# Kernel optimization log

Measured on AMD Instinct MI355X. Metric: run time of the kernel, lower is better.

The kernel has to match this reference:

```python
import jax, jax.numpy as jnp
import numpy as np

B, N, S, VOCAB, D, NNZ = 16, 2048, 4096, 50257, 128, 1048576


def setup_inputs() -> dict:
    key = jax.random.key(0)
    k1, k2, k3, k4, k5, k6 = jax.random.split(key, 6)
    return {
        "subnode_ids": jax.random.randint(k1, (B, S), 0, VOCAB),
        "mask_batch": jax.random.randint(k2, (NNZ,), 0, B),
        "mask_node": jax.random.randint(k3, (NNZ,), 0, N),
        "mask_subnode": jax.random.randint(k4, (NNZ,), 0, S),
        "mask_values": jax.random.uniform(k5, (NNZ,), dtype=jnp.float32),
        "emb_table": jax.random.normal(k6, (VOCAB, D), dtype=jnp.float32),
    }


def reference(subnode_ids, mask_batch, mask_node, mask_subnode, mask_values, emb_table):
    # Gather token embeddings for every (batch, subnode) slot: [B, S, D] -> [B*S, D]
    subnode_emb = emb_table[subnode_ids].reshape(B * S, D)
    # Flattened COO indices (same as batch*max_nodes + node, batch*max_subnodes + subnode)
    row = mask_batch * N + mask_node      # destination node slot in [0, B*N)
    col = mask_batch * S + mask_subnode   # source subnode slot in [0, B*S)
    # Fused gather + weighted scatter-add (== sparse.mm of expanded_mask @ subnode_emb)
    contrib = subnode_emb[col] * mask_values[:, None]           # [NNZ, D]
    pooled = jax.ops.segment_sum(contrib, row, num_segments=B * N)  # [B*N, D]
    return pooled.reshape(B, N, D)
```

## Files before the change

### kernel.cpp

```cpp
#include <hip/hip_runtime.h>
#include <hip/hip_fp16.h>

#define Bq 16
#define Nq 2048
#define Sq 4096
#define Dq 128
#define VOCABq 50257
#define NNZq 1048576
#define ROWS (Bq * Nq)
#define NBIN 1024
#define RPB 32
#define BCAP 1280
#define OVF_MAX 65536
#define BTPB 1024
#define BEPT 4

typedef unsigned long long u64;
typedef float vfloat4 __attribute__((ext_vector_type(4)));
typedef unsigned short vushort4 __attribute__((ext_vector_type(4)));

__global__ __launch_bounds__(256) void cast_kernel(
    const float* __restrict__ emb, unsigned short* __restrict__ emb16)
{
    const int NQUAD = (VOCABq * Dq) / 4;
    int i = blockIdx.x * 256 + threadIdx.x;
    if (i >= NQUAD) return;
    vfloat4 f = reinterpret_cast<const vfloat4*>(emb)[i];
    vushort4 h;
    h.x = __half_as_ushort(__float2half_rn(f.x));
    h.y = __half_as_ushort(__float2half_rn(f.y));
    h.z = __half_as_ushort(__float2half_rn(f.z));
    h.w = __half_as_ushort(__float2half_rn(f.w));
    __builtin_nontemporal_store(h, reinterpret_cast<vushort4*>(emb16) + i);
}

__global__ __launch_bounds__(BTPB) void bin_kernel(
    const int* __restrict__ subnode_ids,
    const int* __restrict__ mb,
    const int* __restrict__ mn,
    const int* __restrict__ ms,
    const float* __restrict__ mv,
    int* __restrict__ binCnt,
    u64* __restrict__ binMem,
    int* __restrict__ ovfn,
    int* __restrict__ ovf)
{
    __shared__ int hist[NBIN];
    __shared__ int base[NBIN];
    int t = threadIdx.x;
    for (int g = t; g < NBIN; g += BTPB) hist[g] = 0;
    __syncthreads();

    int blockBase = blockIdx.x * (BTPB * BEPT);
    int g[BEPT], rank[BEPT];
    u64 pk[BEPT];
    #pragma unroll
    for (int k = 0; k < BEPT; k++) {
        int i   = blockBase + k * BTPB + t;
        int b   = mb[i];
        int row = b * Nq + mn[i];
        int tok = subnode_ids[b * Sq + ms[i]];
        float v = mv[i];
        g[k]  = row >> 5;
        pk[k] = ((u64)(unsigned)__float_as_int(v) << 32)
              | ((u64)(row & 31) << 16)
              | (unsigned)tok;
        rank[k] = atomicAdd(&hist[g[k]], 1);
    }
    __syncthreads();
    for (int gg = t; gg < NBIN; gg += BTPB) {
        int h = hist[gg];
        base[gg] = h ? atomicAdd(&binCnt[gg], h) : 0;
    }
    __syncthreads();
    #pragma unroll
    for (int k = 0; k < BEPT; k++) {
        int p = base[g[k]] + rank[k];
        if (p < BCAP) {
            binMem[(size_t)g[k] * BCAP + p] = pk[k];
        } else {
            int o = atomicAdd(ovfn, 1);
            if (o < OVF_MAX) ovf[o] = blockBase + k * BTPB + t;
        }
    }
}

__global__ __launch_bounds__(256) void pool_kernel(
    const unsigned short* __restrict__ emb16,
    const int* __restrict__ binCnt,
    const u64* __restrict__ binMem,
    float* __restrict__ out)
{
    __shared__ u64 ebuf[BCAP];
    __shared__ int hist[RPB];
    __shared__ int start[RPB + 1];
    __shared__ int cursor[RPB];

    int t   = threadIdx.x;
    int bin = blockIdx.x;
    if (t < RPB) hist[t] = 0;
    __syncthreads();

    int n = min(binCnt[bin], BCAP);
    const u64* bm = binMem + (size_t)bin * BCAP;

    for (int e = t; e < n; e += 256) {
        int rl = (int)((bm[e] >> 16) & 31);
        atomicAdd(&hist[rl], 1);
    }
    __syncthreads();
    if (t < 32) {
        int v = hist[t];
        #pragma unroll
        for (int d = 1; d < 32; d <<= 1) {
            int w = __shfl_up(v, d, 32);
            if (t >= d) v += w;
        }
        start[t + 1] = v;
        if (t == 0) start[0] = 0;
    }
    __syncthreads();
    if (t < RPB) cursor[t] = start[t];
    __syncthreads();
    for (int e = t; e < n; e += 256) {
        u64 pk = bm[e];
        int rl = (int)((pk >> 16) & 31);
        int p  = atomicAdd(&cursor[rl], 1);
        ebuf[p] = pk;
    }
    __syncthreads();

    int gi   = t >> 5;
    int lane = t & 31;
    for (int rr = 0; rr < 4; rr++) {
        int r  = gi * 4 + rr;
        int s0 = start[r], s1 = start[r + 1];
        vfloat4 acc = {0.f, 0.f, 0.f, 0.f};
        int k = s0;
        for (; k + 8 <= s1; k += 8) {
            int   tk[8];
            float vv[8];
            #pragma unroll
            for (int u = 0; u < 8; u++) {
                u64 pk = ebuf[k + u];
                tk[u] = (int)(pk & 0xFFFF);
                vv[u] = __int_as_float((int)(pk >> 32));
            }
            vushort4 e[8];
            #pragma unroll
            for (int u = 0; u < 8; u++)
                e[u] = reinterpret_cast<const vushort4*>(emb16 + (size_t)tk[u] * Dq)[lane];
            #pragma unroll
            for (int u = 0; u < 8; u++) {
                acc.x += __half2float(__ushort_as_half(e[u].x)) * vv[u];
                acc.y += __half2float(__ushort_as_half(e[u].y)) * vv[u];
                acc.z += __half2float(__ushort_as_half(e[u].z)) * vv[u];
                acc.w += __half2float(__ushort_as_half(e[u].w)) * vv[u];
            }
        }
        for (; k < s1; k++) {
            u64 pk = ebuf[k];
            int   tok = (int)(pk & 0xFFFF);
            float v   = __int_as_float((int)(pk >> 32));
            vushort4 e = reinterpret_cast<const vushort4*>(emb16 + (size_t)tok * Dq)[lane];
            acc.x += __half2float(__ushort_as_half(e.x)) * v;
            acc.y += __half2float(__ushort_as_half(e.y)) * v;
            acc.z += __half2float(__ushort_as_half(e.z)) * v;
            acc.w += __half2float(__ushort_as_half(e.w)) * v;
        }
        __builtin_nontemporal_store(
            acc, reinterpret_cast<vfloat4*>(out + ((size_t)bin * RPB + r) * Dq) + lane);
    }
}

__global__ __launch_bounds__(256) void overflow_kernel(
    const int* __restrict__ subnode_ids,
    const int* __restrict__ mb, const int* __restrict__ mn,
    const int* __restrict__ ms, const float* __restrict__ mv,
    const float* __restrict__ emb,
    const int* __restrict__ ovfn, const int* __restrict__ ovf,
    float* __restrict__ out)
{
    int nov = min(*ovfn, OVF_MAX);
    for (int e = blockIdx.x * 256 + threadIdx.x; e < nov; e += gridDim.x * 256) {
        int i = ovf[e];
        int b = mb[i];
        int row = b * Nq + mn[i];
        int tok = subnode_ids[b * Sq + ms[i]];
        float v = mv[i];
        const float* src = emb + (size_t)tok * Dq;
        float* dst = out + (size_t)row * Dq;
        for (int d = 0; d < Dq; d++) unsafeAtomicAdd(dst + d, src[d] * v);
    }
}

extern "C" void kernel_launch(void* const* d_in, const int* in_sizes, int n_in,
                              void* d_out, int out_size, void* d_ws, size_t ws_size,
                              hipStream_t stream) {
    const int*   subnode_ids  = (const int*)d_in[0];
    const int*   mask_batch   = (const int*)d_in[1];
    const int*   mask_node    = (const int*)d_in[2];
    const int*   mask_subnode = (const int*)d_in[3];
    const float* mask_values  = (const float*)d_in[4];
    const float* emb_table    = (const float*)d_in[5];
    float*       out          = (float*)d_out;

    unsigned short* emb16 = (unsigned short*)d_ws;
    u64* binMem = (u64*)(emb16 + (size_t)VOCABq * Dq + 64 );
    int* binCnt = (int*)(binMem + (size_t)NBIN * BCAP);
    int* ovfn   = binCnt + NBIN;
    int* ovf    = ovfn + 64;

    (void)hipMemsetAsync(binCnt, 0, (NBIN + 64) * sizeof(int), stream);

    const int NQUAD = (VOCABq * Dq) / 4;
    cast_kernel<<<(NQUAD + 255) / 256, 256, 0, stream>>>(emb_table, emb16);
    bin_kernel<<<NNZq / (BTPB * BEPT), BTPB, 0, stream>>>(
        subnode_ids, mask_batch, mask_node, mask_subnode, mask_values,
        binCnt, binMem, ovfn, ovf);
    pool_kernel<<<NBIN, 256, 0, stream>>>(emb16, binCnt, binMem, out);
    overflow_kernel<<<32, 256, 0, stream>>>(
        subnode_ids, mask_batch, mask_node, mask_subnode, mask_values,
        emb_table, ovfn, ovf, out);
}
```

Measured before the change: 143.2 us.

## Halve pool bin size, sort entries by token range, widen gathers to 16B

Bins now cover 16 rows instead of 32, doubling the pool grid to 2048 blocks. Inside each bin, entries are sorted by a (token high bits, row) key so that concurrent groups gather from nearby embedding regions. Each 16-lane group owns one row across the four token quarters. Gathers are widened to 8 halves per lane, and entries are kept in registers so the bin buffer is read from global memory once instead of twice. The change aims to improve occupancy, load width and L2 locality, at the cost of lower bin capacity (768), which could push more entries onto the slow atomic overflow path.

```diff
diff --git a/kernel.cpp b/kernel.cpp
--- a/kernel.cpp
+++ b/kernel.cpp
@@ -8,9 +8,9 @@
 #define VOCABq 50257
 #define NNZq 1048576
 #define ROWS (Bq * Nq)
-#define NBIN 1024
-#define RPB 32
-#define BCAP 1280
+#define NBIN 2048
+#define RPB 16
+#define BCAP 768
 #define OVF_MAX 65536
 #define BTPB 1024
 #define BEPT 4
@@ -18,6 +18,7 @@
 typedef unsigned long long u64;
 typedef float vfloat4 __attribute__((ext_vector_type(4)));
 typedef unsigned short vushort4 __attribute__((ext_vector_type(4)));
+typedef unsigned short vushort8 __attribute__((ext_vector_type(8)));
 
 __global__ __launch_bounds__(256) void cast_kernel(
     const float* __restrict__ emb, unsigned short* __restrict__ emb16)
@@ -61,9 +62,9 @@
         int row = b * Nq + mn[i];
         int tok = subnode_ids[b * Sq + ms[i]];
         float v = mv[i];
-        g[k]  = row >> 5;
+        g[k]  = row >> 4;
         pk[k] = ((u64)(unsigned)__float_as_int(v) << 32)
-              | ((u64)(row & 31) << 16)
+              | ((u64)(row & 15) << 16)
               | (unsigned)tok;
         rank[k] = atomicAdd(&hist[g[k]], 1);
     }
@@ -92,50 +93,54 @@
     float* __restrict__ out)
 {
     __shared__ u64 ebuf[BCAP];
-    __shared__ int hist[RPB];
-    __shared__ int start[RPB + 1];
-    __shared__ int cursor[RPB];
+    __shared__ int hist[64];
+    __shared__ int start[65];
+    __shared__ int cursor[64];
 
     int t   = threadIdx.x;
     int bin = blockIdx.x;
-    if (t < RPB) hist[t] = 0;
+    if (t < 64) hist[t] = 0;
     __syncthreads();
 
     int n = min(binCnt[bin], BCAP);
     const u64* bm = binMem + (size_t)bin * BCAP;
 
+    u64 myPk[3];
+    int myKey[3], myCnt = 0;
     for (int e = t; e < n; e += 256) {
-        int rl = (int)((bm[e] >> 16) & 31);
-        atomicAdd(&hist[rl], 1);
-    }
-    __syncthreads();
-    if (t < 32) {
+        u64 pk  = bm[e];
+        int tok = (int)(pk & 0xFFFF);
+        int key = ((tok >> 14) << 4) | (int)((pk >> 16) & 15);
+        myPk[myCnt] = pk; myKey[myCnt] = key; myCnt++;
+        atomicAdd(&hist[key], 1);
+    }
+    __syncthreads();
+    if (t < 64) {
         int v = hist[t];
         #pragma unroll
-        for (int d = 1; d < 32; d <<= 1) {
-            int w = __shfl_up(v, d, 32);
+        for (int d = 1; d < 64; d <<= 1) {
+            int w = __shfl_up(v, d, 64);
             if (t >= d) v += w;
         }
         start[t + 1] = v;
         if (t == 0) start[0] = 0;
     }
     __syncthreads();
-    if (t < RPB) cursor[t] = start[t];
-    __syncthreads();
-    for (int e = t; e < n; e += 256) {
-        u64 pk = bm[e];
-        int rl = (int)((pk >> 16) & 31);
-        int p  = atomicAdd(&cursor[rl], 1);
-        ebuf[p] = pk;
-    }
-    __syncthreads();
-
-    int gi   = t >> 5;
-    int lane = t & 31;
-    for (int rr = 0; rr < 4; rr++) {
-        int r  = gi * 4 + rr;
-        int s0 = start[r], s1 = start[r + 1];
-        vfloat4 acc = {0.f, 0.f, 0.f, 0.f};
+    if (t < 64) cursor[t] = start[t];
+    __syncthreads();
+    for (int k = 0; k < myCnt; k++) {
+        int p = atomicAdd(&cursor[myKey[k]], 1);
+        ebuf[p] = myPk[k];
+    }
+    __syncthreads();
+
+    int g    = t >> 4;
+    int lane = t & 15;
+    vfloat4 a0 = {0.f, 0.f, 0.f, 0.f};
+    vfloat4 a1 = {0.f, 0.f, 0.f, 0.f};
+    #pragma unroll
+    for (int q = 0; q < 4; q++) {
+        int s0 = start[q * 16 + g], s1 = start[q * 16 + g + 1];
         int k = s0;
         for (; k + 8 <= s1; k += 8) {
             int   tk[8];
@@ -146,31 +151,40 @@
                 tk[u] = (int)(pk & 0xFFFF);
                 vv[u] = __int_as_float((int)(pk >> 32));
             }
-            vushort4 e[8];
+            vushort8 e[8];
             #pragma unroll
             for (int u = 0; u < 8; u++)
-                e[u] = reinterpret_cast<const vushort4*>(emb16 + (size_t)tk[u] * Dq)[lane];
+                e[u] = reinterpret_cast<const vushort8*>(emb16 + (size_t)tk[u] * Dq)[lane];
             #pragma unroll
             for (int u = 0; u < 8; u++) {
-                acc.x += __half2float(__ushort_as_half(e[u].x)) * vv[u];
-                acc.y += __half2float(__ushort_as_half(e[u].y)) * vv[u];
-                acc.z += __half2float(__ushort_as_half(e[u].z)) * vv[u];
-                acc.w += __half2float(__ushort_as_half(e[u].w)) * vv[u];
+                a0.x += __half2float(__ushort_as_half(e[u][0])) * vv[u];
+                a0.y += __half2float(__ushort_as_half(e[u][1])) * vv[u];
+                a0.z += __half2float(__ushort_as_half(e[u][2])) * vv[u];
+                a0.w += __half2float(__ushort_as_half(e[u][3])) * vv[u];
+                a1.x += __half2float(__ushort_as_half(e[u][4])) * vv[u];
+                a1.y += __half2float(__ushort_as_half(e[u][5])) * vv[u];
+                a1.z += __half2float(__ushort_as_half(e[u][6])) * vv[u];
+                a1.w += __half2float(__ushort_as_half(e[u][7])) * vv[u];
             }
         }
         for (; k < s1; k++) {
             u64 pk = ebuf[k];
             int   tok = (int)(pk & 0xFFFF);
             float v   = __int_as_float((int)(pk >> 32));
-            vushort4 e = reinterpret_cast<const vushort4*>(emb16 + (size_t)tok * Dq)[lane];
-            acc.x += __half2float(__ushort_as_half(e.x)) * v;
-            acc.y += __half2float(__ushort_as_half(e.y)) * v;
-            acc.z += __half2float(__ushort_as_half(e.z)) * v;
-            acc.w += __half2float(__ushort_as_half(e.w)) * v;
-        }
-        __builtin_nontemporal_store(
-            acc, reinterpret_cast<vfloat4*>(out + ((size_t)bin * RPB + r) * Dq) + lane);
-    }
+            vushort8 e = reinterpret_cast<const vushort8*>(emb16 + (size_t)tok * Dq)[lane];
+            a0.x += __half2float(__ushort_as_half(e[0])) * v;
+            a0.y += __half2float(__ushort_as_half(e[1])) * v;
+            a0.z += __half2float(__ushort_as_half(e[2])) * v;
+            a0.w += __half2float(__ushort_as_half(e[3])) * v;
+            a1.x += __half2float(__ushort_as_half(e[4])) * v;
+            a1.y += __half2float(__ushort_as_half(e[5])) * v;
+            a1.z += __half2float(__ushort_as_half(e[6])) * v;
+            a1.w += __half2float(__ushort_as_half(e[7])) * v;
+        }
+    }
+    float* orow = out + ((size_t)bin * RPB + g) * Dq + lane * 8;
+    __builtin_nontemporal_store(a0, reinterpret_cast<vfloat4*>(orow));
+    __builtin_nontemporal_store(a1, reinterpret_cast<vfloat4*>(orow) + 1);
 }
 
 __global__ __launch_bounds__(256) void overflow_kernel(
```

Result: faster. 137.7 us (-3.9%).
